# Kernel tuning notes

Hardware: AMD Instinct MI355X
Metric: run time of the kernel (lower is better)

The kernel has to match this reference:

```python
import jax, jax.numpy as jnp
import numpy as np

SEQ_LEN = 4096
D_IN = 1024
D_OUT = 1024


def setup_inputs() -> dict:
    key = jax.random.key(0)
    k_x, k_q, k_k, k_v = jax.random.split(key, 4)
    s = 1.0 / np.sqrt(D_IN)
    return {
        "x": jax.random.normal(k_x, (SEQ_LEN, D_IN), dtype=jnp.float32),
        "W_query": jax.random.normal(k_q, (D_IN, D_OUT), dtype=jnp.float32) * s,
        "W_key": jax.random.normal(k_k, (D_IN, D_OUT), dtype=jnp.float32) * s,
        "W_value": jax.random.normal(k_v, (D_IN, D_OUT), dtype=jnp.float32) * s,
    }


def reference(x, W_query, W_key, W_value):
    # QKV projections (Linear without bias): [S, d_out]
    q = x @ W_query
    k = x @ W_key
    v = x @ W_value
    # Full S x S score matrix, causal mask, scaled softmax
    scores = q @ k.T  # [S, S]
    seq_len = x.shape[0]
    causal = jnp.tril(jnp.ones((seq_len, seq_len), dtype=bool))
    scores = jnp.where(causal, scores, -jnp.inf)
    scale = 1.0 / jnp.sqrt(jnp.asarray(k.shape[-1], dtype=scores.dtype))
    attn = jax.nn.softmax(scores * scale, axis=-1)
    return attn @ v  # [S, d_out]
```

## Files before the change

kernel.cpp:

```cpp
#include <hip/hip_runtime.h>
#include <math.h>

#define SEQ 4096
#define DIM 1024

typedef unsigned short u16;
typedef __attribute__((ext_vector_type(8))) short short8;
typedef __attribute__((ext_vector_type(4))) float floatx4;
typedef __attribute__((ext_vector_type(4))) unsigned short us4;

__device__ __forceinline__ float bf2f(u16 u) {
    union { unsigned int i; float f; } c; c.i = ((unsigned int)u) << 16; return c.f;
}
__device__ __forceinline__ u16 f2bf(float f) {
    union { float f; unsigned int i; } c; c.f = f;
    return (u16)((c.i + 0x7fffu + ((c.i >> 16) & 1u)) >> 16);
}
__device__ __forceinline__ void gload_lds16(const u16* g, u16* l) {
    __builtin_amdgcn_global_load_lds((const __attribute__((address_space(1))) void*)g,
                                     (__attribute__((address_space(3))) void*)l, 16, 0, 0);
}

template <int MODE>
__global__ __launch_bounds__(256) void gemm_nt(const u16* __restrict__ A,
                                               const u16* __restrict__ B,
                                               void* __restrict__ Cv,
                                               float* __restrict__ Ppart,
                                               u16* __restrict__ VtOut,
                                               int lda, int ldb, int ldc, int Kdim,
                                               float scale0) {
    const int row0 = blockIdx.y * 128;
    const int col0 = blockIdx.x * 128;
    if (MODE == 1 && col0 > row0) return;
    int kbeg = 0, kend = Kdim, chunk = 0;
    if (MODE == 2) {
        chunk = blockIdx.z;
        kbeg = chunk << 10;
        const int klim = row0 + 128;
        if (kbeg >= klim) return;
        kend = min(kbeg + 1024, klim);
    }

    __shared__ u16 As[2][4096];
    __shared__ u16 Bs[2][4096];

    const int tid  = threadIdx.x;
    const int wave = tid >> 6;
    const int lane = tid & 63;
    const int wm = wave & 1;
    const int wn = wave >> 1;

    const int s0 = wave * 128 + lane;
    const int s1 = s0 + 64;
    const int r0s = s0 >> 2, q0s = ((s0 & 3) ^ ((s0 >> 3) & 3)) * 8;
    const int r1s = s1 >> 2, q1s = ((s1 & 3) ^ ((s1 >> 3) & 3)) * 8;
    const u16* aP0 = A + (size_t)(row0 + r0s) * lda + kbeg + q0s;
    const u16* aP1 = A + (size_t)(row0 + r1s) * lda + kbeg + q1s;
    const u16* bP0 = B + (size_t)(col0 + r0s) * ldb + kbeg + q0s;
    const u16* bP1 = B + (size_t)(col0 + r1s) * ldb + kbeg + q1s;
    const int l0 = wave * 1024;

    floatx4 acc[4][4] = {};
    const int niter = (kend - kbeg) >> 5;
    const int frow = lane & 15;
    const int xq = (((lane >> 4) ^ ((frow >> 1) & 3))) * 8;

    gload_lds16(aP0, &As[0][l0]);
    gload_lds16(aP1, &As[0][l0 + 512]);
    gload_lds16(bP0, &Bs[0][l0]);
    gload_lds16(bP1, &Bs[0][l0 + 512]);
    aP0 += 32; aP1 += 32; bP0 += 32; bP1 += 32;

    for (int it = 0; it < niter; ++it) {
        const int cur = it & 1;
        __syncthreads();
        if (it + 1 < niter) {
            const int nxt = cur ^ 1;
            gload_lds16(aP0, &As[nxt][l0]);
            gload_lds16(aP1, &As[nxt][l0 + 512]);
            gload_lds16(bP0, &Bs[nxt][l0]);
            gload_lds16(bP1, &Bs[nxt][l0 + 512]);
            aP0 += 32; aP1 += 32; bP0 += 32; bP1 += 32;
        }
        __builtin_amdgcn_sched_barrier(0);
        short8 af[4], bfr[4];
#pragma unroll
        for (int t = 0; t < 4; ++t) {
            af[t]  = *(const short8*)&As[cur][(wm * 64 + t * 16 + frow) * 32 + xq];
            bfr[t] = *(const short8*)&Bs[cur][(wn * 64 + t * 16 + frow) * 32 + xq];
        }
#pragma unroll
        for (int mt = 0; mt < 4; ++mt)
#pragma unroll
            for (int nt = 0; nt < 4; ++nt)
                acc[mt][nt] = __builtin_amdgcn_mfma_f32_16x16x32_bf16(
                    af[mt], bfr[nt], acc[mt][nt], 0, 0, 0);
    }

    const int cr = (lane >> 4) * 4;
    const int cc = lane & 15;
    if (MODE == 2) {
        float* dst;
        if (chunk == 0) {
            dst = (float*)Cv;
        } else {
            const ptrdiff_t poff[3] = {0, (ptrdiff_t)3072 * 1024, (ptrdiff_t)5120 * 1024};
            dst = Ppart + poff[chunk - 1] - (ptrdiff_t)(chunk << 10) * 1024;
        }
#pragma unroll
        for (int mt = 0; mt < 4; ++mt)
#pragma unroll
            for (int nt = 0; nt < 4; ++nt)
#pragma unroll
                for (int r = 0; r < 4; ++r) {
                    const int row = row0 + wm * 64 + mt * 16 + cr + r;
                    const int col = col0 + wn * 64 + nt * 16 + cc;
                    dst[(size_t)row * ldc + col] = acc[mt][nt][r];
                }
    } else if (MODE == 0 && col0 >= 2048) {
#pragma unroll
        for (int mt = 0; mt < 4; ++mt)
#pragma unroll
            for (int nt = 0; nt < 4; ++nt) {
                const int row = row0 + wm * 64 + mt * 16 + cr;
                const int col = (col0 - 2048) + wn * 64 + nt * 16 + cc;
                us4 o = { f2bf(acc[mt][nt][0]), f2bf(acc[mt][nt][1]),
                          f2bf(acc[mt][nt][2]), f2bf(acc[mt][nt][3]) };
                *(us4*)&VtOut[(size_t)col * SEQ + row] = o;
            }
    } else {
        u16* dst = (u16*)Cv;
        const float sc = (MODE == 0 && col0 < 1024) ? scale0 : 1.0f;
#pragma unroll
        for (int mt = 0; mt < 4; ++mt)
#pragma unroll
            for (int nt = 0; nt < 4; ++nt)
#pragma unroll
                for (int r = 0; r < 4; ++r) {
                    const int row = row0 + wm * 64 + mt * 16 + cr + r;
                    const int col = col0 + wn * 64 + nt * 16 + cc;
                    dst[(size_t)row * ldc + col] = f2bf(acc[mt][nt][r] * sc);
                }
    }
}

__global__ __launch_bounds__(256) void transpose_cast(const float* __restrict__ W0,
                                                      const float* __restrict__ W1,
                                                      const float* __restrict__ W2,
                                                      u16* __restrict__ Wt) {
    __shared__ float tile[32][33];
    const float* W = (blockIdx.z == 0) ? W0 : (blockIdx.z == 1) ? W1 : W2;
    u16* out = Wt + (size_t)blockIdx.z * DIM * DIM;
    const int bx = blockIdx.x * 32;
    const int by = blockIdx.y * 32;
    const int tx = threadIdx.x & 31;
    const int ty = (threadIdx.x >> 5) * 4;
#pragma unroll
    for (int r = 0; r < 4; ++r)
        tile[ty + r][tx] = W[(size_t)(by + ty + r) * DIM + bx + tx];
    __syncthreads();
#pragma unroll
    for (int r = 0; r < 4; ++r)
        out[(size_t)(bx + ty + r) * DIM + by + tx] = f2bf(tile[tx][ty + r]);
}

__global__ __launch_bounds__(256) void cast_bf16(const float* __restrict__ X,
                                                 u16* __restrict__ Xb) {
    const size_t i = ((size_t)blockIdx.x * 256 + threadIdx.x) * 4;
    const float4 v = *(const float4*)(X + i);
    us4 o = { f2bf(v.x), f2bf(v.y), f2bf(v.z), f2bf(v.w) };
    *(us4*)(Xb + i) = o;
}

__global__ __launch_bounds__(256) void softmax_causal_bf16(u16* __restrict__ S) {
    __shared__ float red[4];
    __shared__ float bc;
    const int i = blockIdx.x;
    u16* row = S + (size_t)i * SEQ;
    const int n = i + 1;
    const int tid = threadIdx.x;
    const int zend = (i & ~127) + 128;

    float v[16];
    float m = -3.4e38f;
#pragma unroll
    for (int t = 0; t < 16; ++t) {
        const int j = tid + (t << 8);
        if (j < n) { v[t] = bf2f(row[j]); m = fmaxf(m, v[t]); }
    }
#pragma unroll
    for (int o = 32; o > 0; o >>= 1) m = fmaxf(m, __shfl_down(m, o));
    if ((tid & 63) == 0) red[tid >> 6] = m;
    __syncthreads();
    if (tid == 0) bc = fmaxf(fmaxf(red[0], red[1]), fmaxf(red[2], red[3]));
    __syncthreads();
    m = bc;

    float s = 0.f;
#pragma unroll
    for (int t = 0; t < 16; ++t) {
        const int j = tid + (t << 8);
        if (j < n) { v[t] = __expf(v[t] - m); s += v[t]; }
    }
#pragma unroll
    for (int o = 32; o > 0; o >>= 1) s += __shfl_down(s, o);
    if ((tid & 63) == 0) red[tid >> 6] = s;
    __syncthreads();
    if (tid == 0) bc = 1.0f / (red[0] + red[1] + red[2] + red[3]);
    __syncthreads();
    const float inv = bc;

#pragma unroll
    for (int t = 0; t < 16; ++t) {
        const int j = tid + (t << 8);
        if (j < n) row[j] = f2bf(v[t] * inv);
        else if (j < zend) row[j] = 0;
    }
}

__global__ __launch_bounds__(256) void reduce_pv(float* __restrict__ O,
                                                 const float* __restrict__ P) {
    const int r = blockIdx.x;
    const int row = 1024 + r;
    const int col = threadIdx.x * 4;
    float4 a = *(const float4*)(O + (size_t)row * 1024 + col);
    const float4 b1 = *(const float4*)(P + (size_t)r * 1024 + col);
    a.x += b1.x; a.y += b1.y; a.z += b1.z; a.w += b1.w;
    if (row >= 2048) {
        const float4 b2 = *(const float4*)(P + (size_t)3072 * 1024 +
                                           (size_t)(row - 2048) * 1024 + col);
        a.x += b2.x; a.y += b2.y; a.z += b2.z; a.w += b2.w;
    }
    if (row >= 3072) {
        const float4 b3 = *(const float4*)(P + (size_t)5120 * 1024 +
                                           (size_t)(row - 3072) * 1024 + col);
        a.x += b3.x; a.y += b3.y; a.z += b3.z; a.w += b3.w;
    }
    *(float4*)(O + (size_t)row * 1024 + col) = a;
}

extern "C" void kernel_launch(void* const* d_in, const int* in_sizes, int n_in,
                              void* d_out, int out_size, void* d_ws, size_t ws_size,
                              hipStream_t stream) {
    const float* x  = (const float*)d_in[0];
    const float* Wq = (const float*)d_in[1];
    const float* Wk = (const float*)d_in[2];
    const float* Wv = (const float*)d_in[3];

    u16* xb    = (u16*)d_ws;
    u16* Wt    = xb  + (size_t)SEQ * DIM;
    u16* QK    = Wt  + (size_t)3072 * DIM;
    u16* Vt    = QK  + (size_t)SEQ * 2048;
    u16* S     = Vt  + (size_t)DIM * SEQ;
    float* Ppart = (float*)(S + (size_t)SEQ * SEQ);

    cast_bf16<<<SEQ * DIM / 1024, 256, 0, stream>>>(x, xb);
    transpose_cast<<<dim3(32, 32, 3), 256, 0, stream>>>(Wq, Wk, Wv, Wt);

    gemm_nt<0><<<dim3(24, 32), 256, 0, stream>>>(
        xb, Wt, QK, nullptr, Vt, DIM, DIM, 2048, DIM, 0.03125f);

    gemm_nt<1><<<dim3(32, 32), 256, 0, stream>>>(
        QK, QK + 1024, S, nullptr, nullptr, 2048, 2048, SEQ, DIM, 1.0f);

    softmax_causal_bf16<<<SEQ, 256, 0, stream>>>(S);

    gemm_nt<2><<<dim3(8, 32, 4), 256, 0, stream>>>(
        S, Vt, d_out, Ppart, nullptr, SEQ, SEQ, DIM, SEQ, 1.0f);

    reduce_pv<<<3072, 256, 0, stream>>>((float*)d_out, Ppart);
}
```

Before: 224.6 us.

## Triple-buffer LDS tiles in GEMM with two loads in flight

Moves the GEMM main loop from double to triple LDS buffering so two K-tiles of global-to-LDS loads stay outstanding, with explicit s_waitcnt vmcnt(4) plus s_barrier replacing __syncthreads. Each iteration's prefetch is issued after the fragment reads from the current buffer, which hides more global memory latency behind the MFMA work. The cost is 50% more shared memory per block, which may reduce occupancy. The loop assumes niter >= 2 and depends on the hand-written waitcnt counts being right.

```diff
diff --git a/kernel.cpp b/kernel.cpp
--- a/kernel.cpp
+++ b/kernel.cpp
@@ -41,8 +41,8 @@
         kend = min(kbeg + 1024, klim);
     }
 
-    __shared__ u16 As[2][4096];
-    __shared__ u16 Bs[2][4096];
+    __shared__ u16 As[3][4096];
+    __shared__ u16 Bs[3][4096];
 
     const int tid  = threadIdx.x;
     const int wave = tid >> 6;
@@ -70,24 +70,18 @@
     gload_lds16(bP0, &Bs[0][l0]);
     gload_lds16(bP1, &Bs[0][l0 + 512]);
     aP0 += 32; aP1 += 32; bP0 += 32; bP1 += 32;
-
-    for (int it = 0; it < niter; ++it) {
-        const int cur = it & 1;
-        __syncthreads();
-        if (it + 1 < niter) {
-            const int nxt = cur ^ 1;
-            gload_lds16(aP0, &As[nxt][l0]);
-            gload_lds16(aP1, &As[nxt][l0 + 512]);
-            gload_lds16(bP0, &Bs[nxt][l0]);
-            gload_lds16(bP1, &Bs[nxt][l0 + 512]);
-            aP0 += 32; aP1 += 32; bP0 += 32; bP1 += 32;
-        }
-        __builtin_amdgcn_sched_barrier(0);
+    gload_lds16(aP0, &As[1][l0]);
+    gload_lds16(aP1, &As[1][l0 + 512]);
+    gload_lds16(bP0, &Bs[1][l0]);
+    gload_lds16(bP1, &Bs[1][l0 + 512]);
+    aP0 += 32; aP1 += 32; bP0 += 32; bP1 += 32;
+
+    auto compute_tile = [&](int c) {
         short8 af[4], bfr[4];
 #pragma unroll
         for (int t = 0; t < 4; ++t) {
-            af[t]  = *(const short8*)&As[cur][(wm * 64 + t * 16 + frow) * 32 + xq];
-            bfr[t] = *(const short8*)&Bs[cur][(wn * 64 + t * 16 + frow) * 32 + xq];
+            af[t]  = *(const short8*)&As[c][(wm * 64 + t * 16 + frow) * 32 + xq];
+            bfr[t] = *(const short8*)&Bs[c][(wn * 64 + t * 16 + frow) * 32 + xq];
         }
 #pragma unroll
         for (int mt = 0; mt < 4; ++mt)
@@ -95,7 +89,38 @@
             for (int nt = 0; nt < 4; ++nt)
                 acc[mt][nt] = __builtin_amdgcn_mfma_f32_16x16x32_bf16(
                     af[mt], bfr[nt], acc[mt][nt], 0, 0, 0);
-    }
+    };
+
+    int cur = 0, pre = 2;
+    for (int it = 0; it < niter - 2; ++it) {
+        asm volatile("s_waitcnt vmcnt(4)\n\ts_barrier" ::: "memory");
+        {
+            short8 af[4], bfr[4];
+#pragma unroll
+            for (int t = 0; t < 4; ++t) {
+                af[t]  = *(const short8*)&As[cur][(wm * 64 + t * 16 + frow) * 32 + xq];
+                bfr[t] = *(const short8*)&Bs[cur][(wn * 64 + t * 16 + frow) * 32 + xq];
+            }
+            gload_lds16(aP0, &As[pre][l0]);
+            gload_lds16(aP1, &As[pre][l0 + 512]);
+            gload_lds16(bP0, &Bs[pre][l0]);
+            gload_lds16(bP1, &Bs[pre][l0 + 512]);
+            aP0 += 32; aP1 += 32; bP0 += 32; bP1 += 32;
+#pragma unroll
+            for (int mt = 0; mt < 4; ++mt)
+#pragma unroll
+                for (int nt = 0; nt < 4; ++nt)
+                    acc[mt][nt] = __builtin_amdgcn_mfma_f32_16x16x32_bf16(
+                        af[mt], bfr[nt], acc[mt][nt], 0, 0, 0);
+        }
+        cur = (cur == 2) ? 0 : cur + 1;
+        pre = (pre == 2) ? 0 : pre + 1;
+    }
+    asm volatile("s_waitcnt vmcnt(4)\n\ts_barrier" ::: "memory");
+    compute_tile(cur);
+    cur = (cur == 2) ? 0 : cur + 1;
+    asm volatile("s_waitcnt vmcnt(0)\n\ts_barrier" ::: "memory");
+    compute_tile(cur);
 
     const int cr = (lane >> 4) * 4;
     const int cc = lane & 15;
```

After: 211.1 us. -6.0%, faster.
